# Performance work log

Measured on AMD Instinct MI355X. Metric: run time of the kernel, lower is better.

Reference implementation:

```python
import jax, jax.numpy as jnp
import numpy as np

DIM = 2048
N_HEADS = 32
N_KV_HEADS = 8
HEAD_DIM = DIM // N_HEADS  # 64
GROUP = N_HEADS // N_KV_HEADS  # 4
ROPE_BASE = 10000.0


def setup_inputs() -> dict:
    key = jax.random.key(0)
    k1, k2, k3, k4, k5 = jax.random.split(key, 5)
    b, s = 1, 2048
    scale = 1.0 / np.sqrt(DIM)
    return {
        "x": jax.random.normal(k1, (b, s, DIM), dtype=jnp.float32),
        # weights stored as (in, out); equivalent math to torch Linear (x @ W.T)
        "wq": jax.random.normal(k2, (DIM, N_HEADS * HEAD_DIM), dtype=jnp.float32) * scale,
        "wk": jax.random.normal(k3, (DIM, N_KV_HEADS * HEAD_DIM), dtype=jnp.float32) * scale,
        "wv": jax.random.normal(k4, (DIM, N_KV_HEADS * HEAD_DIM), dtype=jnp.float32) * scale,
        "wo": jax.random.normal(k5, (N_HEADS * HEAD_DIM, DIM), dtype=jnp.float32) * scale,
    }


def _rope_cos_sin(seq_len, dtype):
    inv_freq = 1.0 / (ROPE_BASE ** (jnp.arange(0, HEAD_DIM, 2, dtype=jnp.float32) / HEAD_DIM))
    t = jnp.arange(seq_len, dtype=jnp.float32)
    freqs = jnp.outer(t, inv_freq)              # [s, hd/2]
    emb = jnp.concatenate([freqs, freqs], -1)   # [s, hd]
    return jnp.cos(emb).astype(dtype), jnp.sin(emb).astype(dtype)


def _rotate_half(x):
    x1, x2 = x[..., : HEAD_DIM // 2], x[..., HEAD_DIM // 2 :]
    return jnp.concatenate([-x2, x1], axis=-1)


def reference(x, wq, wk, wv, wo):
    b, s, _ = x.shape
    q = (x @ wq).reshape(b, s, N_HEADS, HEAD_DIM)
    k = (x @ wk).reshape(b, s, N_KV_HEADS, HEAD_DIM)
    v = (x @ wv).reshape(b, s, N_KV_HEADS, HEAD_DIM)

    cos, sin = _rope_cos_sin(s, x.dtype)
    cos = cos[None, :, None, :]  # [1, s, 1, hd] broadcast over batch & heads
    sin = sin[None, :, None, :]
    q = q * cos + _rotate_half(q) * sin
    k = k * cos + _rotate_half(k) * sin

    # GQA: repeat KV heads (repeat_interleave along head dim)
    k = jnp.repeat(k, GROUP, axis=2)  # [b, s, n_heads, hd]
    v = jnp.repeat(v, GROUP, axis=2)

    q = q.transpose(0, 2, 1, 3)  # [b, h, s, d]
    k = k.transpose(0, 2, 1, 3)
    v = v.transpose(0, 2, 1, 3)

    scores = jnp.einsum("bhqd,bhkd->bhqk", q, k) / jnp.sqrt(jnp.asarray(HEAD_DIM, x.dtype))
    attn = jax.nn.softmax(scores, axis=-1)
    out = jnp.einsum("bhqk,bhkd->bhqd", attn, v)
    out = out.transpose(0, 2, 1, 3).reshape(b, s, N_HEADS * HEAD_DIM)
    return out @ wo
```

## Files before the change

kernel.cpp:

```cpp
#include <hip/hip_runtime.h>
#include <hip/hip_bf16.h>

typedef __bf16 bf16x8 __attribute__((ext_vector_type(8)));
typedef __bf16 bf16x4 __attribute__((ext_vector_type(4)));
typedef __bf16 bf16x2 __attribute__((ext_vector_type(2)));
typedef float fx4 __attribute__((ext_vector_type(4)));
typedef float fx16 __attribute__((ext_vector_type(16)));

#define AS1 __attribute__((address_space(1)))
#define AS3 __attribute__((address_space(3)))

__global__ __launch_bounds__(256) void prep(const float4* __restrict__ X, __bf16* __restrict__ Xb,
                                            const float* __restrict__ wq, const float* __restrict__ wk,
                                            const float* __restrict__ wv, const float* __restrict__ wo,
                                            __bf16* __restrict__ WqkvT, __bf16* __restrict__ WoT) {
    const int bx = blockIdx.x;
    if (bx < 4096) {
        const int i = bx * 256 + threadIdx.x;
        const float4 v = X[i];
        bf16x4 o = { (__bf16)v.x, (__bf16)v.y, (__bf16)v.z, (__bf16)v.w };
        *(bf16x4*)(Xb + (size_t)i * 4) = o;
        return;
    }
    constexpr int K = 2048;
    __shared__ float t[64][65];
    const int tt = bx - 4096;
    const float* W; __bf16* Wt; int N, loc;
    if (tt < 1024)      { W = wq; Wt = WqkvT;                       N = 2048; loc = tt; }
    else if (tt < 1280) { W = wk; Wt = WqkvT + (size_t)2048 * 2048; N = 512;  loc = tt - 1024; }
    else if (tt < 1536) { W = wv; Wt = WqkvT + (size_t)2560 * 2048; N = 512;  loc = tt - 1280; }
    else                { W = wo; Wt = WoT;                         N = 2048; loc = tt - 1536; }
    const int k0 = (loc & 31) * 64, n0 = (loc >> 5) * 64;
    const int tx = threadIdx.x & 15, ty = threadIdx.x >> 4;
#pragma unroll
    for (int p = 0; p < 4; ++p) {
        const float4 v = *(const float4*)&W[(size_t)(k0 + p * 16 + ty) * N + n0 + tx * 4];
        t[p * 16 + ty][tx * 4 + 0] = v.x;
        t[p * 16 + ty][tx * 4 + 1] = v.y;
        t[p * 16 + ty][tx * 4 + 2] = v.z;
        t[p * 16 + ty][tx * 4 + 3] = v.w;
    }
    __syncthreads();
#pragma unroll
    for (int p = 0; p < 4; ++p) {
        const int nn = p * 16 + ty;
        bf16x4 o = { (__bf16)t[tx * 4 + 0][nn], (__bf16)t[tx * 4 + 1][nn],
                     (__bf16)t[tx * 4 + 2][nn], (__bf16)t[tx * 4 + 3][nn] };
        *(bf16x4*)&Wt[(size_t)(n0 + nn) * K + k0 + tx * 4] = o;
    }
}

#define GL(p, d) __builtin_amdgcn_global_load_lds((const AS1 void*)(p), (AS3 void*)(d), 16, 0, 0)
#define WBAR(N)  asm volatile("s_waitcnt vmcnt(" #N ") lgkmcnt(0)" ::: "memory");             \
                 __builtin_amdgcn_s_barrier();                                                \
                 __builtin_amdgcn_sched_barrier(0)

#define GEMM_SETUP(Aptr, Btptr)                                                              \
    constexpr int K = 2048;                                                                  \
    __shared__ __align__(16) __bf16 sm[3][8192];                                  \
    const int tid = threadIdx.x;                                                             \
    const int wave = tid >> 6, lane = tid & 63;                                              \
    const int quad = lane >> 4, l16 = lane & 15;                                             \
    const int wm = (wave >> 1) * 64, wn = (wave & 1) * 64;                                   \
    fx4 acc[4][4] = {};                                                                      \
    const int r4 = lane >> 2;                                                                \
    const int c8s = ((lane & 3) ^ ((r4 >> 1) & 3)) * 8;                                      \
    const __bf16* csrc[4]; int cdst[4];                                                      \
    _Pragma("unroll")                                                                        \
    for (int it = 0; it < 4; ++it) {                                                         \
        const int idx = wave * 4 + it;                                                       \
        if (idx < 8) { csrc[it] = (Aptr) + (size_t)(m0 + idx * 16 + r4) * K + c8s;           \
                       cdst[it] = idx * 512 + lane * 8; }                                    \
        else         { csrc[it] = (Btptr) + (size_t)(n0 + (idx - 8) * 16 + r4) * K + c8s;    \
                       cdst[it] = 4096 + (idx - 8) * 512 + lane * 8; }                       \
    }                                                                                        \
    const int colr = (quad ^ ((l16 >> 1) & 3)) * 8;                                          \
    const int arow = (wm + l16) * 32 + colr;                                                 \
    const int brow = 4096 + (wn + l16) * 32 + colr;                                          \
    auto compute = [&](const __bf16* cb) {                                                   \
        bf16x8 af[4], bfr[4];                                                                \
        _Pragma("unroll") for (int i = 0; i < 4; ++i) af[i]  = *(const bf16x8*)&cb[arow + i * 512]; \
        _Pragma("unroll") for (int j = 0; j < 4; ++j) bfr[j] = *(const bf16x8*)&cb[brow + j * 512]; \
        __builtin_amdgcn_s_setprio(1);                                                       \
        _Pragma("unroll") for (int i = 0; i < 4; ++i)                                        \
            _Pragma("unroll") for (int j = 0; j < 4; ++j)                                    \
                acc[i][j] = __builtin_amdgcn_mfma_f32_16x16x32_bf16(af[i], bfr[j], acc[i][j], 0, 0, 0); \
        __builtin_amdgcn_s_setprio(0);                                                       \
    };                                                                                       \
    _Pragma("unroll")                                                                        \
    for (int pt = 0; pt < 2; ++pt)                                                           \
        _Pragma("unroll")                                                                    \
        for (int it = 0; it < 4; ++it)                                                       \
            GL(csrc[it] + pt * 32, &sm[pt][cdst[it]]);                                       \
    _Pragma("unroll 1")                                                                      \
    for (int tq = 0; tq < 20; ++tq) {                                                        \
        _Pragma("unroll")                                                                    \
        for (int u = 0; u < 3; ++u) {                                                        \
            const int t = tq * 3 + u;                                                        \
            WBAR(4);                                                                         \
            const int kofs = (t + 2) * 32;                                                   \
            _Pragma("unroll")                                                                \
            for (int it = 0; it < 4; ++it)                                                   \
                GL(csrc[it] + kofs, &sm[(u + 2) % 3][cdst[it]]);                             \
            compute(sm[u]);                                                                  \
        }                                                                                    \
    }                                                                                        \
    { WBAR(4); _Pragma("unroll") for (int it = 0; it < 4; ++it)                              \
          GL(csrc[it] + 62 * 32, &sm[2][cdst[it]]); compute(sm[0]); }              \
    { WBAR(4); _Pragma("unroll") for (int it = 0; it < 4; ++it)                              \
          GL(csrc[it] + 63 * 32, &sm[0][cdst[it]]); compute(sm[1]); }              \
    { WBAR(4); compute(sm[2]); }                                                   \
    { WBAR(0); compute(sm[0]); }

__global__ __launch_bounds__(256, 3) void gemm_qkv(const __bf16* __restrict__ A, const __bf16* __restrict__ Bt,
                                                   __bf16* __restrict__ Qr, __bf16* __restrict__ Kr,
                                                   __bf16* __restrict__ Vt) {
    const int bid = blockIdx.x;
    const int swz = (bid & 7) * 48 + (bid >> 3);
    const int m0 = (swz & 15) * 128, n0 = (swz >> 4) * 128;

    GEMM_SETUP(A, Bt)

    const int col64 = n0 + wn;
    if (col64 < 2560) {
        const bool isQ = col64 < 2048;
        const float scale = isQ ? 0.18033688011112042f : 1.0f;
        __bf16* base = isQ ? (Qr + (size_t)(col64 >> 6) * 2048 * 64)
                           : (Kr + (size_t)((col64 - 2048) >> 6) * 2048 * 64);
#pragma unroll
        for (int jj = 0; jj < 2; ++jj) {
            const int dlo = jj * 16 + l16;
            const float inv = __builtin_amdgcn_exp2f(-(float)dlo * 0.41524101186092029f);
#pragma unroll
            for (int i = 0; i < 4; ++i)
#pragma unroll
                for (int r = 0; r < 4; ++r) {
                    const int s = m0 + wm + i * 16 + quad * 4 + r;
                    float sn, cs;
                    __sincosf((float)s * inv, &sn, &cs);
                    const float lo = acc[i][jj][r], hv = acc[i][jj + 2][r];
                    base[(size_t)s * 64 + dlo]      = (__bf16)((lo * cs - hv * sn) * scale);
                    base[(size_t)s * 64 + dlo + 32] = (__bf16)((hv * cs + lo * sn) * scale);
                }
        }
    } else {
        __bf16* vb = Vt + (size_t)((col64 - 2560) >> 6) * 64 * 2048;
#pragma unroll
        for (int i = 0; i < 4; ++i)
#pragma unroll
            for (int j = 0; j < 4; ++j) {
                const int d = j * 16 + l16;
                const int s0 = m0 + wm + i * 16 + quad * 4;
                bf16x4 p;
#pragma unroll
                for (int r = 0; r < 4; ++r) p[r] = (__bf16)acc[i][j][r];
                *(bf16x4*)&vb[(size_t)d * 2048 + s0] = p;
            }
    }
}

__global__ __launch_bounds__(256, 3) void gemm_out(const __bf16* __restrict__ A, const __bf16* __restrict__ Bt,
                                                   float* __restrict__ C) {
    const int bid = blockIdx.x;
    const int swz = (bid & 7) * 32 + (bid >> 3);
    const int m0 = (swz & 15) * 128, n0 = (swz >> 4) * 128;

    GEMM_SETUP(A, Bt)

#pragma unroll
    for (int i = 0; i < 4; ++i)
#pragma unroll
        for (int j = 0; j < 4; ++j) {
            const int row = m0 + wm + i * 16 + quad * 4;
            const int col = n0 + wn + j * 16 + l16;
#pragma unroll
            for (int r = 0; r < 4; ++r)
                C[(size_t)(row + r) * 2048 + col] = acc[i][j][r];
        }
}

__global__ __launch_bounds__(512, 4) void flash_attn(const __bf16* __restrict__ Qr, const __bf16* __restrict__ Kr,
                                                     const __bf16* __restrict__ Vt, __bf16* __restrict__ O) {
    constexpr int S = 2048;
    __shared__ __align__(16) __bf16 smem[2][4 * 64 * 72];
    const int qt = blockIdx.x, h = blockIdx.y, kvh = h >> 2;
    const int tid = threadIdx.x, wave = tid >> 6, lane = tid & 63;
    const int grp = wave >> 2, w4 = wave & 3;
    const int l32 = lane & 31, hi = lane >> 5;
    const int goff = grp * 2 * 4608;

    const int qrow = qt * 128 + w4 * 32 + l32;
    const __bf16* qptr = Qr + ((size_t)h * S + qrow) * 64;
    bf16x8 qf[4];
#pragma unroll
    for (int kc = 0; kc < 4; ++kc) qf[kc] = *(const bf16x8*)(qptr + kc * 16 + hi * 8);

    const __bf16* Kbase = Kr + (size_t)kvh * S * 64;
    const __bf16* Vbase = Vt + (size_t)kvh * 64 * S;

    const int gtid = tid & 255;
    const int krow = gtid >> 3;
    const int kcol = (gtid & 7) * 8;
    const int vslot = (kcol & 48) | ((kcol & 8) >> 1);

    bf16x8 kreg0 = *(const bf16x8*)(Kbase + (size_t)(grp * 64 + krow) * 64 + kcol);
    bf16x8 kreg1 = *(const bf16x8*)(Kbase + (size_t)(grp * 64 + 32 + krow) * 64 + kcol);
    bf16x8 vreg0 = *(const bf16x8*)(Vbase + (size_t)krow * S + grp * 64 + kcol);
    bf16x8 vreg1 = *(const bf16x8*)(Vbase + (size_t)(32 + krow) * S + grp * 64 + kcol);

    fx16 ov0, ov1;
#pragma unroll
    for (int i = 0; i < 16; ++i) { ov0[i] = 0.f; ov1[i] = 0.f; }
    float l_acc = 0.f;

    {
        __bf16* nK = &smem[0][goff];
        __bf16* nV = nK + 4608;
        *(bf16x8*)&nK[krow * 72 + kcol] = kreg0;
        *(bf16x8*)&nK[(32 + krow) * 72 + kcol] = kreg1;
        bf16x4 v0lo = { vreg0[0], vreg0[1], vreg0[2], vreg0[3] };
        bf16x4 v0hi = { vreg0[4], vreg0[5], vreg0[6], vreg0[7] };
        bf16x4 v1lo = { vreg1[0], vreg1[1], vreg1[2], vreg1[3] };
        bf16x4 v1hi = { vreg1[4], vreg1[5], vreg1[6], vreg1[7] };
        *(bf16x4*)&nV[krow * 72 + vslot]            = v0lo;
        *(bf16x4*)&nV[krow * 72 + vslot + 8]        = v0hi;
        *(bf16x4*)&nV[(32 + krow) * 72 + vslot]     = v1lo;
        *(bf16x4*)&nV[(32 + krow) * 72 + vslot + 8] = v1hi;
        const int kt1 = 2 + grp;
        kreg0 = *(const bf16x8*)(Kbase + (size_t)(kt1 * 64 + krow) * 64 + kcol);
        kreg1 = *(const bf16x8*)(Kbase + (size_t)(kt1 * 64 + 32 + krow) * 64 + kcol);
        vreg0 = *(const bf16x8*)(Vbase + (size_t)krow * S + kt1 * 64 + kcol);
        vreg1 = *(const bf16x8*)(Vbase + (size_t)(32 + krow) * S + kt1 * 64 + kcol);
    }
    asm volatile("s_waitcnt lgkmcnt(0)" ::: "memory");
    __builtin_amdgcn_s_barrier();
    __builtin_amdgcn_sched_barrier(0);

    for (int it = 0; it < 16; ++it) {
        __bf16* lKg = &smem[it & 1][goff];
        __bf16* lVg = lKg + 4608;

        if (it + 1 < 16) {
            __bf16* nK = &smem[(it + 1) & 1][goff];
            __bf16* nV = nK + 4608;
            *(bf16x8*)&nK[krow * 72 + kcol] = kreg0;
            *(bf16x8*)&nK[(32 + krow) * 72 + kcol] = kreg1;
            bf16x4 v0lo = { vreg0[0], vreg0[1], vreg0[2], vreg0[3] };
            bf16x4 v0hi = { vreg0[4], vreg0[5], vreg0[6], vreg0[7] };
            bf16x4 v1lo = { vreg1[0], vreg1[1], vreg1[2], vreg1[3] };
            bf16x4 v1hi = { vreg1[4], vreg1[5], vreg1[6], vreg1[7] };
            *(bf16x4*)&nV[krow * 72 + vslot]            = v0lo;
            *(bf16x4*)&nV[krow * 72 + vslot + 8]        = v0hi;
            *(bf16x4*)&nV[(32 + krow) * 72 + vslot]     = v1lo;
            *(bf16x4*)&nV[(32 + krow) * 72 + vslot + 8] = v1hi;
            const int it2 = (it + 2 < 16) ? it + 2 : 15;
            const int ktn = it2 * 2 + grp;
            kreg0 = *(const bf16x8*)(Kbase + (size_t)(ktn * 64 + krow) * 64 + kcol);
            kreg1 = *(const bf16x8*)(Kbase + (size_t)(ktn * 64 + 32 + krow) * 64 + kcol);
            vreg0 = *(const bf16x8*)(Vbase + (size_t)krow * S + ktn * 64 + kcol);
            vreg1 = *(const bf16x8*)(Vbase + (size_t)(32 + krow) * S + ktn * 64 + kcol);
        }

        fx16 sc0, sc1;
#pragma unroll
        for (int i = 0; i < 16; ++i) { sc0[i] = 0.f; sc1[i] = 0.f; }
        __builtin_amdgcn_s_setprio(1);
#pragma unroll
        for (int kc = 0; kc < 4; ++kc) {
            const bf16x8 a0 = *(const bf16x8*)&lKg[l32 * 72 + kc * 16 + hi * 8];
            const bf16x8 a1 = *(const bf16x8*)&lKg[(32 + l32) * 72 + kc * 16 + hi * 8];
            sc0 = __builtin_amdgcn_mfma_f32_32x32x16_bf16(a0, qf[kc], sc0, 0, 0, 0);
            sc1 = __builtin_amdgcn_mfma_f32_32x32x16_bf16(a1, qf[kc], sc1, 0, 0, 0);
        }
        __builtin_amdgcn_s_setprio(0);

#pragma unroll
        for (int h2 = 0; h2 < 2; ++h2) {
#pragma unroll
            for (int c = 0; c < 2; ++c) {
                bf16x8 pb; float ps[8];
#pragma unroll
                for (int j = 0; j < 8; ++j) {
                    const float sv = h2 ? sc1[c * 8 + j] : sc0[c * 8 + j];
                    ps[j] = __builtin_amdgcn_exp2f(sv);
                    pb[j] = (__bf16)ps[j];
                }
                l_acc += ((ps[0] + ps[1]) + (ps[2] + ps[3]))
                       + ((ps[4] + ps[5]) + (ps[6] + ps[7]));
                const int kcv = h2 * 2 + c;
                const bf16x8 va0 = *(const bf16x8*)&lVg[l32 * 72 + kcv * 16 + hi * 8];
                const bf16x8 va1 = *(const bf16x8*)&lVg[(32 + l32) * 72 + kcv * 16 + hi * 8];
                __builtin_amdgcn_s_setprio(1);
                ov0 = __builtin_amdgcn_mfma_f32_32x32x16_bf16(va0, pb, ov0, 0, 0, 0);
                ov1 = __builtin_amdgcn_mfma_f32_32x32x16_bf16(va1, pb, ov1, 0, 0, 0);
                __builtin_amdgcn_s_setprio(0);
            }
        }
        asm volatile("s_waitcnt lgkmcnt(0)" ::: "memory");
        __builtin_amdgcn_s_barrier();
        __builtin_amdgcn_sched_barrier(0);
    }

    const float l_pair = l_acc + __shfl_xor(l_acc, 32, 64);

    fx4* lO = (fx4*)&smem[0][0];
    float* lL = (float*)(&smem[0][0] + 16384);
    if (grp == 1) {
#pragma unroll
        for (int ic = 0; ic < 4; ++ic) {
            fx4 c0, c1;
#pragma unroll
            for (int r = 0; r < 4; ++r) { c0[r] = ov0[ic * 4 + r]; c1[r] = ov1[ic * 4 + r]; }
            lO[(ic * 4 + w4) * 64 + lane] = c0;
            lO[((ic + 4) * 4 + w4) * 64 + lane] = c1;
        }
        if (hi == 0) lL[w4 * 32 + l32] = l_pair;
    }
    __syncthreads();
    if (grp == 0) {
#pragma unroll
        for (int ic = 0; ic < 4; ++ic) {
            const fx4 c0 = lO[(ic * 4 + w4) * 64 + lane];
            const fx4 c1 = lO[((ic + 4) * 4 + w4) * 64 + lane];
#pragma unroll
            for (int r = 0; r < 4; ++r) { ov0[ic * 4 + r] += c0[r]; ov1[ic * 4 + r] += c1[r]; }
        }
        const float inv_l = 1.0f / (l_pair + lL[w4 * 32 + l32]);
#pragma unroll
        for (int dt = 0; dt < 2; ++dt)
#pragma unroll
            for (int rg2 = 0; rg2 < 4; ++rg2) {
                bf16x4 o4;
#pragma unroll
                for (int r = 0; r < 4; ++r)
                    o4[r] = (__bf16)((dt ? ov1[rg2 * 4 + r] : ov0[rg2 * 4 + r]) * inv_l);
                const int col = h * 64 + dt * 32 + rg2 * 8 + hi * 4;
                *(bf16x4*)(O + (size_t)qrow * 2048 + col) = o4;
            }
    }
}

extern "C" void kernel_launch(void* const* d_in, const int* in_sizes, int n_in,
                              void* d_out, int out_size, void* d_ws, size_t ws_size,
                              hipStream_t stream) {
    const float* x  = (const float*)d_in[0];
    const float* wq = (const float*)d_in[1];
    const float* wk = (const float*)d_in[2];
    const float* wv = (const float*)d_in[3];
    const float* wo = (const float*)d_in[4];
    float* out = (float*)d_out;
    char* ws = (char*)d_ws;

    __bf16* Xb    = (__bf16*)ws;
    __bf16* WqkvT = (__bf16*)(ws + ((size_t)8 << 20));
    __bf16* WoT   = (__bf16*)(ws + ((size_t)20 << 20));
    __bf16* Qr    = (__bf16*)(ws + ((size_t)28 << 20));
    __bf16* Kr    = (__bf16*)(ws + ((size_t)36 << 20));
    __bf16* Vt    = (__bf16*)(ws + ((size_t)38 << 20));
    __bf16* Ob    = (__bf16*)(ws + ((size_t)40 << 20));

    prep<<<4096 + 2560, 256, 0, stream>>>((const float4*)x, Xb, wq, wk, wv, wo, WqkvT, WoT);
    gemm_qkv<<<384, 256, 0, stream>>>(Xb, WqkvT, Qr, Kr, Vt);
    flash_attn<<<dim3(16, 32), 512, 0, stream>>>(Qr, Kr, Vt, Ob);
    gemm_out<<<256, 256, 0, stream>>>(Ob, WoT, out);
}
```

Measured before the change: 201.4 us.

## Software-pipeline QK^T of next tile with PV of current tile, remap blocks by KV head

Restructures the flash attention loop so that the score MFMAs for the next KV tile are issued in the same phase as the softmax/PV work for the current tile, using two alternating score register sets and a manually unrolled pair of iterations. The grid is also flattened to 1D with block IDs mapped so that consecutive blocks share a KV head, which is meant to improve L2 locality of K/V across XCDs. The aim is to hide exp/convert latency behind matrix work. In exchange it adds a second barrier per iteration and more live registers, which may raise register pressure.

```diff
diff --git a/kernel.cpp b/kernel.cpp
--- a/kernel.cpp
+++ b/kernel.cpp
@@ -183,7 +183,11 @@
                                                      const __bf16* __restrict__ Vt, __bf16* __restrict__ O) {
     constexpr int S = 2048;
     __shared__ __align__(16) __bf16 smem[2][4 * 64 * 72];
-    const int qt = blockIdx.x, h = blockIdx.y, kvh = h >> 2;
+    const int bid = blockIdx.x;
+    const int o = bid >> 3;
+    const int kvh = bid & 7;
+    const int h = kvh * 4 + (o & 3);
+    const int qt = o >> 2;
     const int tid = threadIdx.x, wave = tid >> 6, lane = tid & 63;
     const int grp = wave >> 2, w4 = wave & 3;
     const int l32 = lane & 31, hi = lane >> 5;
@@ -203,108 +207,111 @@
     const int kcol = (gtid & 7) * 8;
     const int vslot = (kcol & 48) | ((kcol & 8) >> 1);
 
-    bf16x8 kreg0 = *(const bf16x8*)(Kbase + (size_t)(grp * 64 + krow) * 64 + kcol);
-    bf16x8 kreg1 = *(const bf16x8*)(Kbase + (size_t)(grp * 64 + 32 + krow) * 64 + kcol);
-    bf16x8 vreg0 = *(const bf16x8*)(Vbase + (size_t)krow * S + grp * 64 + kcol);
-    bf16x8 vreg1 = *(const bf16x8*)(Vbase + (size_t)(32 + krow) * S + grp * 64 + kcol);
+    bf16x8 kreg0, kreg1, vreg0, vreg1;
+
+#define LOADREGS(ITN) do {                                                            \
+        const int ktn_ = (ITN) * 2 + grp;                                             \
+        kreg0 = *(const bf16x8*)(Kbase + (size_t)(ktn_ * 64 + krow) * 64 + kcol);     \
+        kreg1 = *(const bf16x8*)(Kbase + (size_t)(ktn_ * 64 + 32 + krow) * 64 + kcol);\
+        vreg0 = *(const bf16x8*)(Vbase + (size_t)krow * S + ktn_ * 64 + kcol);        \
+        vreg1 = *(const bf16x8*)(Vbase + (size_t)(32 + krow) * S + ktn_ * 64 + kcol); \
+    } while (0)
+
+#define STAGEB(BUF) do {                                                              \
+        __bf16* nK = &smem[BUF][goff];                                                \
+        __bf16* nV = nK + 4608;                                                       \
+        *(bf16x8*)&nK[krow * 72 + kcol] = kreg0;                                      \
+        *(bf16x8*)&nK[(32 + krow) * 72 + kcol] = kreg1;                               \
+        bf16x4 v0lo = { vreg0[0], vreg0[1], vreg0[2], vreg0[3] };                     \
+        bf16x4 v0hi = { vreg0[4], vreg0[5], vreg0[6], vreg0[7] };                     \
+        bf16x4 v1lo = { vreg1[0], vreg1[1], vreg1[2], vreg1[3] };                     \
+        bf16x4 v1hi = { vreg1[4], vreg1[5], vreg1[6], vreg1[7] };                     \
+        *(bf16x4*)&nV[krow * 72 + vslot]            = v0lo;                           \
+        *(bf16x4*)&nV[krow * 72 + vslot + 8]        = v0hi;                           \
+        *(bf16x4*)&nV[(32 + krow) * 72 + vslot]     = v1lo;                           \
+        *(bf16x4*)&nV[(32 + krow) * 72 + vslot + 8] = v1hi;                           \
+    } while (0)
+
+#define QKST(D0, D1, LKG) do {                                                        \
+        _Pragma("unroll") for (int i_ = 0; i_ < 16; ++i_) { (D0)[i_] = 0.f; (D1)[i_] = 0.f; } \
+        __builtin_amdgcn_s_setprio(1);                                                \
+        _Pragma("unroll")                                                             \
+        for (int kc = 0; kc < 4; ++kc) {                                              \
+            const bf16x8 a0 = *(const bf16x8*)&(LKG)[l32 * 72 + kc * 16 + hi * 8];    \
+            const bf16x8 a1 = *(const bf16x8*)&(LKG)[(32 + l32) * 72 + kc * 16 + hi * 8]; \
+            (D0) = __builtin_amdgcn_mfma_f32_32x32x16_bf16(a0, qf[kc], (D0), 0, 0, 0);\
+            (D1) = __builtin_amdgcn_mfma_f32_32x32x16_bf16(a1, qf[kc], (D1), 0, 0, 0);\
+        }                                                                             \
+        __builtin_amdgcn_s_setprio(0);                                                \
+    } while (0)
+
+#define PVPH(LVG, S0, S1) do {                                                        \
+        _Pragma("unroll")                                                             \
+        for (int h2 = 0; h2 < 2; ++h2) {                                              \
+            _Pragma("unroll")                                                         \
+            for (int c = 0; c < 2; ++c) {                                             \
+                bf16x8 pb; float ps[8];                                               \
+                _Pragma("unroll")                                                     \
+                for (int j = 0; j < 8; ++j) {                                         \
+                    const float sv = h2 ? (S1)[c * 8 + j] : (S0)[c * 8 + j];          \
+                    ps[j] = __builtin_amdgcn_exp2f(sv);                               \
+                    pb[j] = (__bf16)ps[j];                                            \
+                }                                                                     \
+                l_acc += ((ps[0] + ps[1]) + (ps[2] + ps[3]))                          \
+                       + ((ps[4] + ps[5]) + (ps[6] + ps[7]));                         \
+                const int kcv = h2 * 2 + c;                                           \
+                const bf16x8 va0 = *(const bf16x8*)&(LVG)[l32 * 72 + kcv * 16 + hi * 8]; \
+                const bf16x8 va1 = *(const bf16x8*)&(LVG)[(32 + l32) * 72 + kcv * 16 + hi * 8]; \
+                __builtin_amdgcn_s_setprio(1);                                        \
+                ov0 = __builtin_amdgcn_mfma_f32_32x32x16_bf16(va0, pb, ov0, 0, 0, 0); \
+                ov1 = __builtin_amdgcn_mfma_f32_32x32x16_bf16(va1, pb, ov1, 0, 0, 0); \
+                __builtin_amdgcn_s_setprio(0);                                        \
+            }                                                                         \
+        }                                                                             \
+    } while (0)
+
+#define LGKMBAR() do {                                                                \
+        asm volatile("s_waitcnt lgkmcnt(0)" ::: "memory");                            \
+        __builtin_amdgcn_s_barrier();                                                 \
+        __builtin_amdgcn_sched_barrier(0);                                            \
+    } while (0)
+
+#define FITER(IT, BUFR, BUFW, SCP0, SCP1, SCQ0, SCQ1) do {                            \
+        STAGEB(BUFW);                                                                 \
+        LOADREGS(((IT) + 2 < 16) ? (IT) + 2 : 15);                                    \
+        LGKMBAR();                                                                    \
+        PVPH(&smem[BUFR][goff] + 4608, SCP0, SCP1);                                   \
+        QKST(SCQ0, SCQ1, &smem[BUFW][goff]);                                          \
+        LGKMBAR();                                                                    \
+    } while (0)
 
     fx16 ov0, ov1;
 #pragma unroll
     for (int i = 0; i < 16; ++i) { ov0[i] = 0.f; ov1[i] = 0.f; }
     float l_acc = 0.f;
 
-    {
-        __bf16* nK = &smem[0][goff];
-        __bf16* nV = nK + 4608;
-        *(bf16x8*)&nK[krow * 72 + kcol] = kreg0;
-        *(bf16x8*)&nK[(32 + krow) * 72 + kcol] = kreg1;
-        bf16x4 v0lo = { vreg0[0], vreg0[1], vreg0[2], vreg0[3] };
-        bf16x4 v0hi = { vreg0[4], vreg0[5], vreg0[6], vreg0[7] };
-        bf16x4 v1lo = { vreg1[0], vreg1[1], vreg1[2], vreg1[3] };
-        bf16x4 v1hi = { vreg1[4], vreg1[5], vreg1[6], vreg1[7] };
-        *(bf16x4*)&nV[krow * 72 + vslot]            = v0lo;
-        *(bf16x4*)&nV[krow * 72 + vslot + 8]        = v0hi;
-        *(bf16x4*)&nV[(32 + krow) * 72 + vslot]     = v1lo;
-        *(bf16x4*)&nV[(32 + krow) * 72 + vslot + 8] = v1hi;
-        const int kt1 = 2 + grp;
-        kreg0 = *(const bf16x8*)(Kbase + (size_t)(kt1 * 64 + krow) * 64 + kcol);
-        kreg1 = *(const bf16x8*)(Kbase + (size_t)(kt1 * 64 + 32 + krow) * 64 + kcol);
-        vreg0 = *(const bf16x8*)(Vbase + (size_t)krow * S + kt1 * 64 + kcol);
-        vreg1 = *(const bf16x8*)(Vbase + (size_t)(32 + krow) * S + kt1 * 64 + kcol);
-    }
-    asm volatile("s_waitcnt lgkmcnt(0)" ::: "memory");
-    __builtin_amdgcn_s_barrier();
-    __builtin_amdgcn_sched_barrier(0);
-
-    for (int it = 0; it < 16; ++it) {
-        __bf16* lKg = &smem[it & 1][goff];
-        __bf16* lVg = lKg + 4608;
-
-        if (it + 1 < 16) {
-            __bf16* nK = &smem[(it + 1) & 1][goff];
-            __bf16* nV = nK + 4608;
-            *(bf16x8*)&nK[krow * 72 + kcol] = kreg0;
-            *(bf16x8*)&nK[(32 + krow) * 72 + kcol] = kreg1;
-            bf16x4 v0lo = { vreg0[0], vreg0[1], vreg0[2], vreg0[3] };
-            bf16x4 v0hi = { vreg0[4], vreg0[5], vreg0[6], vreg0[7] };
-            bf16x4 v1lo = { vreg1[0], vreg1[1], vreg1[2], vreg1[3] };
-            bf16x4 v1hi = { vreg1[4], vreg1[5], vreg1[6], vreg1[7] };
-            *(bf16x4*)&nV[krow * 72 + vslot]            = v0lo;
-            *(bf16x4*)&nV[krow * 72 + vslot + 8]        = v0hi;
-            *(bf16x4*)&nV[(32 + krow) * 72 + vslot]     = v1lo;
-            *(bf16x4*)&nV[(32 + krow) * 72 + vslot + 8] = v1hi;
-            const int it2 = (it + 2 < 16) ? it + 2 : 15;
-            const int ktn = it2 * 2 + grp;
-            kreg0 = *(const bf16x8*)(Kbase + (size_t)(ktn * 64 + krow) * 64 + kcol);
-            kreg1 = *(const bf16x8*)(Kbase + (size_t)(ktn * 64 + 32 + krow) * 64 + kcol);
-            vreg0 = *(const bf16x8*)(Vbase + (size_t)krow * S + ktn * 64 + kcol);
-            vreg1 = *(const bf16x8*)(Vbase + (size_t)(32 + krow) * S + ktn * 64 + kcol);
-        }
-
-        fx16 sc0, sc1;
-#pragma unroll
-        for (int i = 0; i < 16; ++i) { sc0[i] = 0.f; sc1[i] = 0.f; }
-        __builtin_amdgcn_s_setprio(1);
-#pragma unroll
-        for (int kc = 0; kc < 4; ++kc) {
-            const bf16x8 a0 = *(const bf16x8*)&lKg[l32 * 72 + kc * 16 + hi * 8];
-            const bf16x8 a1 = *(const bf16x8*)&lKg[(32 + l32) * 72 + kc * 16 + hi * 8];
-            sc0 = __builtin_amdgcn_mfma_f32_32x32x16_bf16(a0, qf[kc], sc0, 0, 0, 0);
-            sc1 = __builtin_amdgcn_mfma_f32_32x32x16_bf16(a1, qf[kc], sc1, 0, 0, 0);
-        }
-        __builtin_amdgcn_s_setprio(0);
-
-#pragma unroll
-        for (int h2 = 0; h2 < 2; ++h2) {
-#pragma unroll
-            for (int c = 0; c < 2; ++c) {
-                bf16x8 pb; float ps[8];
-#pragma unroll
-                for (int j = 0; j < 8; ++j) {
-                    const float sv = h2 ? sc1[c * 8 + j] : sc0[c * 8 + j];
-                    ps[j] = __builtin_amdgcn_exp2f(sv);
-                    pb[j] = (__bf16)ps[j];
-                }
-                l_acc += ((ps[0] + ps[1]) + (ps[2] + ps[3]))
-                       + ((ps[4] + ps[5]) + (ps[6] + ps[7]));
-                const int kcv = h2 * 2 + c;
-                const bf16x8 va0 = *(const bf16x8*)&lVg[l32 * 72 + kcv * 16 + hi * 8];
-                const bf16x8 va1 = *(const bf16x8*)&lVg[(32 + l32) * 72 + kcv * 16 + hi * 8];
-                __builtin_amdgcn_s_setprio(1);
-                ov0 = __builtin_amdgcn_mfma_f32_32x32x16_bf16(va0, pb, ov0, 0, 0, 0);
-                ov1 = __builtin_amdgcn_mfma_f32_32x32x16_bf16(va1, pb, ov1, 0, 0, 0);
-                __builtin_amdgcn_s_setprio(0);
-            }
-        }
-        asm volatile("s_waitcnt lgkmcnt(0)" ::: "memory");
-        __builtin_amdgcn_s_barrier();
-        __builtin_amdgcn_sched_barrier(0);
-    }
+    LOADREGS(0);
+    STAGEB(0);
+    LOADREGS(1);
+    LGKMBAR();
+
+    fx16 scA0, scA1, scB0, scB1;
+    QKST(scA0, scA1, &smem[0][goff]);
+    LGKMBAR();
+
+#pragma unroll 1
+    for (int t = 0; t < 7; ++t) {
+        FITER(2 * t,     0, 1, scA0, scA1, scB0, scB1);
+        FITER(2 * t + 1, 1, 0, scB0, scB1, scA0, scA1);
+    }
+    FITER(14, 0, 1, scA0, scA1, scB0, scB1);
+    PVPH(&smem[1][goff] + 4608, scB0, scB1);
 
     const float l_pair = l_acc + __shfl_xor(l_acc, 32, 64);
 
     fx4* lO = (fx4*)&smem[0][0];
     float* lL = (float*)(&smem[0][0] + 16384);
+    __syncthreads();
     if (grp == 1) {
 #pragma unroll
         for (int ic = 0; ic < 4; ++ic) {
@@ -338,6 +345,12 @@
                 *(bf16x4*)(O + (size_t)qrow * 2048 + col) = o4;
             }
     }
+#undef LOADREGS
+#undef STAGEB
+#undef QKST
+#undef PVPH
+#undef LGKMBAR
+#undef FITER
 }
 
 extern "C" void kernel_launch(void* const* d_in, const int* in_sizes, int n_in,
@@ -361,6 +374,6 @@
 
     prep<<<4096 + 2560, 256, 0, stream>>>((const float4*)x, Xb, wq, wk, wv, wo, WqkvT, WoT);
     gemm_qkv<<<384, 256, 0, stream>>>(Xb, WqkvT, Qr, Kr, Vt);
-    flash_attn<<<dim3(16, 32), 512, 0, stream>>>(Qr, Kr, Vt, Ob);
+    flash_attn<<<512, 512, 0, stream>>>(Qr, Kr, Vt, Ob);
     gemm_out<<<256, 256, 0, stream>>>(Ob, WoT, out);
 }
```

Measured after the change: 222.7 us. +10.6%, slower.

## Drop split-KV wave groups in flash attention, use 4 waves over full KV

Applied to the files above, without the earlier changes.

The attention kernel previously ran 8 waves per block, split into two groups that each handled half of the KV tiles, and merged the two partial outputs through shared memory at the end. It now runs 4 waves per block, each iterating over all 32 KV tiles, which removes the cross-group reduction, the extra sync, and half of the LDS footprint. The trade-off is half as many waves in flight per block and a serial KV loop twice as long. Higher block occupancy from the smaller LDS use may or may not make up for that.

```diff
diff --git a/kernel.cpp b/kernel.cpp
--- a/kernel.cpp
+++ b/kernel.cpp
@@ -179,17 +179,15 @@
         }
 }
 
-__global__ __launch_bounds__(512, 4) void flash_attn(const __bf16* __restrict__ Qr, const __bf16* __restrict__ Kr,
+__global__ __launch_bounds__(256, 4) void flash_attn(const __bf16* __restrict__ Qr, const __bf16* __restrict__ Kr,
                                                      const __bf16* __restrict__ Vt, __bf16* __restrict__ O) {
     constexpr int S = 2048;
-    __shared__ __align__(16) __bf16 smem[2][4 * 64 * 72];
+    __shared__ __align__(16) __bf16 smem[2][2 * 4608];
     const int qt = blockIdx.x, h = blockIdx.y, kvh = h >> 2;
     const int tid = threadIdx.x, wave = tid >> 6, lane = tid & 63;
-    const int grp = wave >> 2, w4 = wave & 3;
     const int l32 = lane & 31, hi = lane >> 5;
-    const int goff = grp * 2 * 4608;
-
-    const int qrow = qt * 128 + w4 * 32 + l32;
+
+    const int qrow = qt * 128 + wave * 32 + l32;
     const __bf16* qptr = Qr + ((size_t)h * S + qrow) * 64;
     bf16x8 qf[4];
 #pragma unroll
@@ -198,67 +196,54 @@
     const __bf16* Kbase = Kr + (size_t)kvh * S * 64;
     const __bf16* Vbase = Vt + (size_t)kvh * 64 * S;
 
-    const int gtid = tid & 255;
-    const int krow = gtid >> 3;
-    const int kcol = (gtid & 7) * 8;
+    const int krow = tid >> 3;
+    const int kcol = (tid & 7) * 8;
     const int vslot = (kcol & 48) | ((kcol & 8) >> 1);
 
-    bf16x8 kreg0 = *(const bf16x8*)(Kbase + (size_t)(grp * 64 + krow) * 64 + kcol);
-    bf16x8 kreg1 = *(const bf16x8*)(Kbase + (size_t)(grp * 64 + 32 + krow) * 64 + kcol);
-    bf16x8 vreg0 = *(const bf16x8*)(Vbase + (size_t)krow * S + grp * 64 + kcol);
-    bf16x8 vreg1 = *(const bf16x8*)(Vbase + (size_t)(32 + krow) * S + grp * 64 + kcol);
+    bf16x8 kreg0, kreg1, vreg0, vreg1;
+
+#define LOADREGS(KT) do {                                                             \
+        const size_t co = (size_t)(KT) * 64;                                          \
+        kreg0 = *(const bf16x8*)(Kbase + (co + krow) * 64 + kcol);                    \
+        kreg1 = *(const bf16x8*)(Kbase + (co + 32 + krow) * 64 + kcol);               \
+        vreg0 = *(const bf16x8*)(Vbase + (size_t)krow * S + co + kcol);               \
+        vreg1 = *(const bf16x8*)(Vbase + (size_t)(32 + krow) * S + co + kcol);        \
+    } while (0)
+
+#define STAGEB(BUF) do {                                                              \
+        __bf16* nK = &smem[BUF][0];                                                   \
+        __bf16* nV = nK + 4608;                                                       \
+        *(bf16x8*)&nK[krow * 72 + kcol] = kreg0;                                      \
+        *(bf16x8*)&nK[(32 + krow) * 72 + kcol] = kreg1;                               \
+        bf16x4 v0lo = { vreg0[0], vreg0[1], vreg0[2], vreg0[3] };                     \
+        bf16x4 v0hi = { vreg0[4], vreg0[5], vreg0[6], vreg0[7] };                     \
+        bf16x4 v1lo = { vreg1[0], vreg1[1], vreg1[2], vreg1[3] };                     \
+        bf16x4 v1hi = { vreg1[4], vreg1[5], vreg1[6], vreg1[7] };                     \
+        *(bf16x4*)&nV[krow * 72 + vslot]            = v0lo;                           \
+        *(bf16x4*)&nV[krow * 72 + vslot + 8]        = v0hi;                           \
+        *(bf16x4*)&nV[(32 + krow) * 72 + vslot]     = v1lo;                           \
+        *(bf16x4*)&nV[(32 + krow) * 72 + vslot + 8] = v1hi;                           \
+    } while (0)
 
     fx16 ov0, ov1;
 #pragma unroll
     for (int i = 0; i < 16; ++i) { ov0[i] = 0.f; ov1[i] = 0.f; }
     float l_acc = 0.f;
 
-    {
-        __bf16* nK = &smem[0][goff];
-        __bf16* nV = nK + 4608;
-        *(bf16x8*)&nK[krow * 72 + kcol] = kreg0;
-        *(bf16x8*)&nK[(32 + krow) * 72 + kcol] = kreg1;
-        bf16x4 v0lo = { vreg0[0], vreg0[1], vreg0[2], vreg0[3] };
-        bf16x4 v0hi = { vreg0[4], vreg0[5], vreg0[6], vreg0[7] };
-        bf16x4 v1lo = { vreg1[0], vreg1[1], vreg1[2], vreg1[3] };
-        bf16x4 v1hi = { vreg1[4], vreg1[5], vreg1[6], vreg1[7] };
-        *(bf16x4*)&nV[krow * 72 + vslot]            = v0lo;
-        *(bf16x4*)&nV[krow * 72 + vslot + 8]        = v0hi;
-        *(bf16x4*)&nV[(32 + krow) * 72 + vslot]     = v1lo;
-        *(bf16x4*)&nV[(32 + krow) * 72 + vslot + 8] = v1hi;
-        const int kt1 = 2 + grp;
-        kreg0 = *(const bf16x8*)(Kbase + (size_t)(kt1 * 64 + krow) * 64 + kcol);
-        kreg1 = *(const bf16x8*)(Kbase + (size_t)(kt1 * 64 + 32 + krow) * 64 + kcol);
-        vreg0 = *(const bf16x8*)(Vbase + (size_t)krow * S + kt1 * 64 + kcol);
-        vreg1 = *(const bf16x8*)(Vbase + (size_t)(32 + krow) * S + kt1 * 64 + kcol);
-    }
+    LOADREGS(0);
+    STAGEB(0);
+    LOADREGS(1);
     asm volatile("s_waitcnt lgkmcnt(0)" ::: "memory");
     __builtin_amdgcn_s_barrier();
     __builtin_amdgcn_sched_barrier(0);
 
-    for (int it = 0; it < 16; ++it) {
-        __bf16* lKg = &smem[it & 1][goff];
-        __bf16* lVg = lKg + 4608;
-
-        if (it + 1 < 16) {
-            __bf16* nK = &smem[(it + 1) & 1][goff];
-            __bf16* nV = nK + 4608;
-            *(bf16x8*)&nK[krow * 72 + kcol] = kreg0;
-            *(bf16x8*)&nK[(32 + krow) * 72 + kcol] = kreg1;
-            bf16x4 v0lo = { vreg0[0], vreg0[1], vreg0[2], vreg0[3] };
-            bf16x4 v0hi = { vreg0[4], vreg0[5], vreg0[6], vreg0[7] };
-            bf16x4 v1lo = { vreg1[0], vreg1[1], vreg1[2], vreg1[3] };
-            bf16x4 v1hi = { vreg1[4], vreg1[5], vreg1[6], vreg1[7] };
-            *(bf16x4*)&nV[krow * 72 + vslot]            = v0lo;
-            *(bf16x4*)&nV[krow * 72 + vslot + 8]        = v0hi;
-            *(bf16x4*)&nV[(32 + krow) * 72 + vslot]     = v1lo;
-            *(bf16x4*)&nV[(32 + krow) * 72 + vslot + 8] = v1hi;
-            const int it2 = (it + 2 < 16) ? it + 2 : 15;
-            const int ktn = it2 * 2 + grp;
-            kreg0 = *(const bf16x8*)(Kbase + (size_t)(ktn * 64 + krow) * 64 + kcol);
-            kreg1 = *(const bf16x8*)(Kbase + (size_t)(ktn * 64 + 32 + krow) * 64 + kcol);
-            vreg0 = *(const bf16x8*)(Vbase + (size_t)krow * S + ktn * 64 + kcol);
-            vreg1 = *(const bf16x8*)(Vbase + (size_t)(32 + krow) * S + ktn * 64 + kcol);
+    for (int it = 0; it < 32; ++it) {
+        const __bf16* lKg = &smem[it & 1][0];
+        const __bf16* lVg = lKg + 4608;
+
+        if (it + 1 < 32) {
+            STAGEB((it + 1) & 1);
+            LOADREGS((it + 2 < 32) ? it + 2 : 31);
         }
 
         fx16 sc0, sc1;
@@ -302,42 +287,21 @@
     }
 
     const float l_pair = l_acc + __shfl_xor(l_acc, 32, 64);
-
-    fx4* lO = (fx4*)&smem[0][0];
-    float* lL = (float*)(&smem[0][0] + 16384);
-    if (grp == 1) {
-#pragma unroll
-        for (int ic = 0; ic < 4; ++ic) {
-            fx4 c0, c1;
-#pragma unroll
-            for (int r = 0; r < 4; ++r) { c0[r] = ov0[ic * 4 + r]; c1[r] = ov1[ic * 4 + r]; }
-            lO[(ic * 4 + w4) * 64 + lane] = c0;
-            lO[((ic + 4) * 4 + w4) * 64 + lane] = c1;
-        }
-        if (hi == 0) lL[w4 * 32 + l32] = l_pair;
-    }
-    __syncthreads();
-    if (grp == 0) {
-#pragma unroll
-        for (int ic = 0; ic < 4; ++ic) {
-            const fx4 c0 = lO[(ic * 4 + w4) * 64 + lane];
-            const fx4 c1 = lO[((ic + 4) * 4 + w4) * 64 + lane];
-#pragma unroll
-            for (int r = 0; r < 4; ++r) { ov0[ic * 4 + r] += c0[r]; ov1[ic * 4 + r] += c1[r]; }
-        }
-        const float inv_l = 1.0f / (l_pair + lL[w4 * 32 + l32]);
-#pragma unroll
-        for (int dt = 0; dt < 2; ++dt)
-#pragma unroll
-            for (int rg2 = 0; rg2 < 4; ++rg2) {
-                bf16x4 o4;
-#pragma unroll
-                for (int r = 0; r < 4; ++r)
-                    o4[r] = (__bf16)((dt ? ov1[rg2 * 4 + r] : ov0[rg2 * 4 + r]) * inv_l);
-                const int col = h * 64 + dt * 32 + rg2 * 8 + hi * 4;
-                *(bf16x4*)(O + (size_t)qrow * 2048 + col) = o4;
-            }
-    }
+    const float inv_l = 1.0f / l_pair;
+
+#pragma unroll
+    for (int dt = 0; dt < 2; ++dt)
+#pragma unroll
+        for (int rg2 = 0; rg2 < 4; ++rg2) {
+            bf16x4 o4;
+#pragma unroll
+            for (int r = 0; r < 4; ++r)
+                o4[r] = (__bf16)((dt ? ov1[rg2 * 4 + r] : ov0[rg2 * 4 + r]) * inv_l);
+            const int col = h * 64 + dt * 32 + rg2 * 8 + hi * 4;
+            *(bf16x4*)(O + (size_t)qrow * 2048 + col) = o4;
+        }
+#undef LOADREGS
+#undef STAGEB
 }
 
 extern "C" void kernel_launch(void* const* d_in, const int* in_sizes, int n_in,
@@ -361,6 +325,6 @@
 
     prep<<<4096 + 2560, 256, 0, stream>>>((const float4*)x, Xb, wq, wk, wv, wo, WqkvT, WoT);
     gemm_qkv<<<384, 256, 0, stream>>>(Xb, WqkvT, Qr, Kr, Vt);
-    flash_attn<<<dim3(16, 32), 512, 0, stream>>>(Qr, Kr, Vt, Ob);
+    flash_attn<<<dim3(16, 32), 256, 0, stream>>>(Qr, Kr, Vt, Ob);
     gemm_out<<<256, 256, 0, stream>>>(Ob, WoT, out);
 }
```

Result: faster. 197.1 us (-2.1%).
